# Performance work log

Measured on AMD Instinct MI355X. Metric: run time of the kernel, lower is better.

## Reference

```python
import jax, jax.numpy as jnp
import numpy as np

N = 100_000      # nodes
E = 500_000      # bonds
DN = 128         # dim_node_embedding
DB = 64          # dim_bond_embedding
NTOK = 4         # num_bond_token
DIN = 2 * DN + 2 * DB  # 384
LEAKY = 0.001
LN_EPS = 1e-5
DIST_MAX = 20.0
STEP = 0.5


def _lrelu(v):
    return jnp.where(v >= 0, v, LEAKY * v)


def _layernorm(v, w, b):
    m = v.mean(-1, keepdims=True)
    var = ((v - m) ** 2).mean(-1, keepdims=True)
    return (v - m) / jnp.sqrt(var + LN_EPS) * w + b


def setup_inputs() -> dict:
    key = jax.random.key(0)
    ks = jax.random.split(key, 20)
    x = jax.random.normal(ks[0], (N, 3), dtype=jnp.float32) * 3.0
    pos = jax.random.normal(ks[1], (N, 3), dtype=jnp.float32)
    node_embedding = jax.random.normal(ks[2], (N, DN), dtype=jnp.float32)
    i0 = jax.random.randint(ks[3], (E,), 0, N)
    off = jax.random.randint(ks[4], (E,), 1, N)  # nonzero -> no self-bonds
    bond_index = jnp.stack([i0, (i0 + off) % N], axis=1).astype(jnp.int32)
    bond_types = jax.random.randint(ks[5], (E,), 0, NTOK).astype(jnp.int32)
    s = 0.02
    params = dict(
        bond_emb=jax.random.normal(ks[6], (NTOK, DB), dtype=jnp.float32),
        W0=jax.random.normal(ks[7], (DIN, DN), dtype=jnp.float32) * s,
        b0=jnp.zeros((DN,), jnp.float32),
        W1=jax.random.normal(ks[8], (DN, DN), dtype=jnp.float32) * s,
        b1=jnp.zeros((DN,), jnp.float32),
        ln1_w=jnp.ones((DN,), jnp.float32),
        ln1_b=jnp.zeros((DN,), jnp.float32),
        W2=jax.random.normal(ks[9], (DN, DN), dtype=jnp.float32) * s,
        b2=jnp.zeros((DN,), jnp.float32),
        ln2_w=jnp.ones((DN,), jnp.float32),
        ln2_b=jnp.zeros((DN,), jnp.float32),
        Wo=jax.random.normal(ks[10], (DN, 2), dtype=jnp.float32) * s,
        bo=jnp.zeros((2,), jnp.float32),
    )
    return dict(x=x, pos=pos, node_embedding=node_embedding,
                bond_index=bond_index, bond_types=bond_types, **params)


def reference(x, pos, node_embedding, bond_index, bond_types,
              bond_emb, W0, b0, W1, b1, ln1_w, ln1_b,
              W2, b2, ln2_w, ln2_b, Wo, bo):
    i = bond_index[:, 0]
    j = bond_index[:, 1]

    # ---- BondLength geometry ----
    diff = x[i] - x[j]                                   # [E,3]
    dist = jnp.linalg.norm(diff, axis=-1, keepdims=True)  # [E,1]
    u = diff / dist                                       # [E,3] unit j->i? (i-j)/d
    direction = jnp.stack([u, -u], axis=-1)               # [E,3,2]

    # ---- Smearing (gaussian RBF + overflow bin, normalized) ----
    offset = jnp.linspace(0.0, DIST_MAX, DB - 1, dtype=jnp.float32)  # [63]
    delta = DIST_MAX / (DB - 2)
    coeff = -0.5 / (delta * delta)
    rbf = jnp.exp(coeff * (dist - offset) ** 2)            # [E,63]
    ovf = (dist >= DIST_MAX).astype(x.dtype)               # [E,1]
    smear = jnp.concatenate([rbf, ovf], axis=-1)           # [E,64]
    smear = smear / smear.sum(axis=-1, keepdims=True)

    # ---- Edge MLP (LeakyMLP, num_layer=2, dim_end=2) ----
    feat = jnp.concatenate(
        [node_embedding[i], node_embedding[j], bond_emb[bond_types], smear],
        axis=-1)                                           # [E,384]
    h = _lrelu(feat @ W0 + b0)
    h = _lrelu(_layernorm(h @ W1 + b1, ln1_w, ln1_b))
    h = _lrelu(_layernorm(h @ W2 + b2, ln2_w, ln2_b))
    force = h @ Wo + bo                                    # [E,2]

    # ---- position update (scatter-add) ----
    update = force[:, None, :] * direction                 # [E,3,2]
    pos = pos.at[i].add(STEP * update[..., 0])
    pos = pos.at[j].add(STEP * update[..., 1])
    return pos
```

## Files before the change

kernel.cpp:

```cpp
#include <hip/hip_runtime.h>
#include <stdint.h>

#define N_EDGES 500000
#define N_NODES 100000
#define PREP_NG 4
#define TBINS 1280

typedef __attribute__((ext_vector_type(8))) short short8;
typedef __attribute__((ext_vector_type(4))) float floatx4;
typedef __attribute__((ext_vector_type(2))) float f32x2;
typedef __attribute__((ext_vector_type(4))) unsigned int u32x4v;
typedef __attribute__((ext_vector_type(2))) int i32x2v;

__device__ __forceinline__ uint16_t f2bf(float f) {
  union { float f; uint32_t u; } cv; cv.f = f;
  uint32_t u = cv.u;
  return (uint16_t)((u + 0x7FFFu + ((u >> 16) & 1u)) >> 16);
}
__device__ __forceinline__ uint32_t pk2bf(float lo, float hi) {
  return __builtin_amdgcn_perm(__float_as_uint(hi), __float_as_uint(lo), 0x07060302u);
}
__device__ __forceinline__ uint16_t bftrunc(float f) {
  return (uint16_t)(__float_as_uint(f) >> 16);
}
__device__ __forceinline__ float lrelu(float v) { return fmaxf(v, 0.001f * v); }

__device__ __forceinline__ f32x2 unpk2(uint32_t u) {
  return (f32x2){ __uint_as_float(u << 16), __uint_as_float(u & 0xFFFF0000u) };
}
__device__ __forceinline__ uint32_t comp2(uint32_t a, uint32_t b, uint32_t t0, uint32_t t1,
                                          f32x2 w2) {
  f32x2 p  = unpk2(a) + unpk2(b);
  f32x2 v0 = unpk2(t0), v1 = unpk2(t1);
  f32x2 r  = p + (v0 + w2 * (v1 - v0));
  f32x2 rl = r * 0.001f;
  return pk2bf(fmaxf(r.x, rl.x), fmaxf(r.y, rl.y));
}
__device__ __forceinline__ floatx4 lrelu4(floatx4 v) {
  floatx4 w = v * 0.001f;
  v.x = fmaxf(v.x, w.x); v.y = fmaxf(v.y, w.y);
  v.z = fmaxf(v.z, w.z); v.w = fmaxf(v.w, w.w);
  return v;
}

__global__ void prep0_kernel(const float* __restrict__ W0, const float* __restrict__ b0,
                             const float* __restrict__ W1, const float* __restrict__ W2,
                             const float* __restrict__ bemb,
                             uint16_t* __restrict__ w0ab, uint16_t* __restrict__ w1f,
                             uint16_t* __restrict__ w2f, float* __restrict__ be0f,
                             const float* __restrict__ pos, float* __restrict__ out, int npos) {
  int id = blockIdx.x * 256 + threadIdx.x;
  if (id < 32768) {
    int f = id;
    int j = f & 7, lane = (f >> 3) & 63, ntt = (f >> 9) & 15, ks = f >> 13;
    int k = ks * 32 + (lane >> 4) * 8 + j;
    int row = (ntt < 8) ? k : (128 + k);
    int col = (ntt & 7) * 16 + (lane & 15);
    w0ab[f] = f2bf(W0[row * 128 + col]);
  } else if (id < 49152) {
    int f = id - 32768;
    int j = f & 7, lane = (f >> 3) & 63, nt = (f >> 9) & 7, ks = f >> 12;
    int k = ks * 32 + (lane >> 4) * 8 + j;
    w1f[f] = f2bf(W1[k * 128 + nt * 16 + (lane & 15)]);
  } else if (id < 65536) {
    int f = id - 49152;
    int j = f & 7, lane = (f >> 3) & 63, nt = (f >> 9) & 7, ks = f >> 12;
    int k = ks * 32 + (lane >> 4) * 8 + j;
    w2f[f] = f2bf(W2[k * 128 + nt * 16 + (lane & 15)]);
  } else if (id < 66048) {
    int t = id - 65536; int ty = t >> 7, n = t & 127;
    float s = b0[n];
    for (int kk = 0; kk < 64; ++kk) s += bemb[ty * 64 + kk] * W0[(256 + kk) * 128 + n];
    be0f[t] = s;
  } else if (id - 66048 < npos) {
    out[id - 66048] = pos[id - 66048];
  }
}

__global__ __attribute__((amdgpu_flat_work_group_size(256, 256)))
void prep_tp_kernel(const float* __restrict__ W0, const float* __restrict__ be0f,
                    uint16_t* __restrict__ T,
                    const float* __restrict__ nemb, const uint16_t* __restrict__ w0ab,
                    uint16_t* __restrict__ Pa, uint16_t* __restrict__ Pb) {
  __shared__ __align__(16) uint16_t aLds[4 * PREP_NG * 16 * 136];
  __shared__ float rbf[64];
  const int tid = threadIdx.x;

  if (blockIdx.x < TBINS) {
    int b = blockIdx.x;
    float dist = (float)b * (1.0f / 32.0f);
    const float delta = 20.0f / 62.0f;
    const float coeff = -0.5f / (delta * delta);
    if (tid < 64) {
      float v;
      if (tid < 63) { float d = dist - (float)tid * delta; v = __expf(coeff * d * d); }
      else v = (dist >= 20.0f) ? 1.0f : 0.0f;
      rbf[tid] = v;
    }
    __syncthreads();
    float sum = 0.0f;
    for (int k = 0; k < 64; ++k) sum += rbf[k];
    float rs = 1.0f / sum;
    for (int o = tid; o < 512; o += 256) {
      int ty = o >> 7, n = o & 127;
      float s = be0f[ty * 128 + n];
      for (int k = 0; k < 64; ++k) s += rbf[k] * rs * W0[(320 + k) * 128 + n];
      T[((size_t)(ty * TBINS + b)) * 128 + n] = f2bf(s);
    }
    return;
  }

  const int pblk = blockIdx.x - TBINS;
  const int lane = tid & 63;
  const int wave = tid >> 6;
  const int n15 = lane & 15;
  const int quad = lane >> 4;
  uint16_t* myA = aLds + wave * (PREP_NG * 16 * 136);
  const int base = pblk * (64 * PREP_NG) + wave * (16 * PREP_NG);

  {
    const int le = lane >> 2, sub = lane & 3;
#pragma unroll
    for (int it = 0; it < PREP_NG; ++it) {
      int r = base + it * 16 + le; if (r >= N_NODES) r = N_NODES - 1;
      const float4* src = (const float4*)(nemb + (size_t)r * 128);
#pragma unroll
      for (int g = 0; g < 4; ++g) {
        float4 a = src[sub * 8 + g * 2], b = src[sub * 8 + g * 2 + 1];
        uint4 pk;
        pk.x = pk2bf(a.x, a.y); pk.y = pk2bf(a.z, a.w);
        pk.z = pk2bf(b.x, b.y); pk.w = pk2bf(b.z, b.w);
        *(uint4*)(myA + (it * 16 + le) * 136 + sub * 32 + g * 8) = pk;
      }
    }
  }

  const short8* wfv = (const short8*)w0ab + lane;
#pragma unroll
  for (int q = 0; q < 4; ++q) {
    short8 bfr[16];
#pragma unroll
    for (int ks = 0; ks < 4; ++ks)
#pragma unroll
      for (int nq = 0; nq < 4; ++nq)
        bfr[ks * 4 + nq] = wfv[(ks * 16 + q * 4 + nq) * 64];
#pragma unroll
    for (int it = 0; it < PREP_NG; ++it) {
      floatx4 acc[4];
#pragma unroll
      for (int nq = 0; nq < 4; ++nq) acc[nq] = (floatx4){0.f, 0.f, 0.f, 0.f};
#pragma unroll
      for (int ks = 0; ks < 4; ++ks) {
        short8 a = *(const short8*)(myA + (it * 16 + n15) * 136 + ks * 32 + quad * 8);
#pragma unroll
        for (int nq = 0; nq < 4; ++nq)
          acc[nq] = __builtin_amdgcn_mfma_f32_16x16x32_bf16(a, bfr[ks * 4 + nq], acc[nq], 0, 0, 0);
      }
      uint16_t* dst = (q < 2) ? Pa : Pb;
      int cbase = ((q & 1) * 4) * 16 + n15;
#pragma unroll
      for (int nq = 0; nq < 4; ++nq) {
        int c = cbase + nq * 16;
#pragma unroll
        for (int r = 0; r < 4; ++r) {
          int row = base + it * 16 + quad * 4 + r;
          if (row < N_NODES) dst[(size_t)row * 128 + c] = bftrunc(acc[nq][r]);
        }
      }
    }
  }
}

__device__ __forceinline__ void gemm_g2(const uint16_t* __restrict__ wf,
                                        const uint16_t* aRow0, const uint16_t* aRow1,
                                        int lane, floatx4* acc0, floatx4* acc1) {
  short8 a0[4], a1[4];
#pragma unroll
  for (int ks = 0; ks < 4; ++ks) {
    a0[ks] = *(const short8*)(aRow0 + ks * 32);
    a1[ks] = *(const short8*)(aRow1 + ks * 32);
  }
  const short8* wv = (const short8*)wf + lane;
#pragma unroll
  for (int ks = 0; ks < 4; ++ks)
#pragma unroll
    for (int nt = 0; nt < 8; ++nt) {
      short8 b = wv[(ks * 8 + nt) * 64];
      acc0[nt] = __builtin_amdgcn_mfma_f32_16x16x32_bf16(a0[ks], b, acc0[nt], 0, 0, 0);
      acc1[nt] = __builtin_amdgcn_mfma_f32_16x16x32_bf16(a1[ks], b, acc1[nt], 0, 0, 0);
    }
}

__device__ __forceinline__ void epilogue1(floatx4* acc, uint16_t* hA, int n15, int quad,
                                          const float* __restrict__ b1,
                                          const float* __restrict__ ln1w,
                                          const float* __restrict__ ln1b) {
  float bv[8], wv[8], bb[8];
#pragma unroll
  for (int nt = 0; nt < 8; ++nt) {
    int col = nt * 16 + n15;
    bv[nt] = b1[col]; wv[nt] = ln1w[col]; bb[nt] = ln1b[col];
  }
  floatx4 s4 = {0.f, 0.f, 0.f, 0.f}, q4 = {0.f, 0.f, 0.f, 0.f};
#pragma unroll
  for (int nt = 0; nt < 8; ++nt) { floatx4 v = acc[nt] + bv[nt]; s4 += v; q4 += v * v; }
#pragma unroll
  for (int m = 1; m <= 8; m <<= 1) {
#pragma unroll
    for (int c = 0; c < 4; ++c) { s4[c] += __shfl_xor(s4[c], m); q4[c] += __shfl_xor(q4[c], m); }
  }
  floatx4 mean = s4 * (1.0f / 128.0f);
  floatx4 var = q4 * (1.0f / 128.0f) - mean * mean;
  floatx4 rstd;
  rstd.x = rsqrtf(var.x + 1e-5f); rstd.y = rsqrtf(var.y + 1e-5f);
  rstd.z = rsqrtf(var.z + 1e-5f); rstd.w = rsqrtf(var.w + 1e-5f);
#pragma unroll
  for (int nt = 0; nt < 8; ++nt) {
    floatx4 v = acc[nt] + bv[nt];
    floatx4 vn = lrelu4((v - mean) * (rstd * wv[nt]) + bb[nt]);
#pragma unroll
    for (int r = 0; r < 4; ++r)
      hA[(quad * 4 + r) * 136 + nt * 16 + n15] = bftrunc(vn[r]);
  }
}

__device__ __forceinline__ void epilogue2(floatx4* acc, int n15, int quad, int edge0, int gr0,
                                          const float (*u_lds)[3], const int (*ij_lds)[2],
                                          const float* __restrict__ b2,
                                          const float* __restrict__ ln2w,
                                          const float* __restrict__ ln2b,
                                          const float* __restrict__ Wo,
                                          const float* __restrict__ bo,
                                          float* __restrict__ out) {
  float bv[8], wv[8], bb[8], wo0[8], wo1[8];
#pragma unroll
  for (int nt = 0; nt < 8; ++nt) {
    int col = nt * 16 + n15;
    bv[nt] = b2[col]; wv[nt] = ln2w[col]; bb[nt] = ln2b[col];
    wo0[nt] = Wo[2 * col]; wo1[nt] = Wo[2 * col + 1];
  }
  floatx4 s4 = {0.f, 0.f, 0.f, 0.f}, q4 = {0.f, 0.f, 0.f, 0.f};
#pragma unroll
  for (int nt = 0; nt < 8; ++nt) { floatx4 v = acc[nt] + bv[nt]; s4 += v; q4 += v * v; }
#pragma unroll
  for (int m = 1; m <= 8; m <<= 1) {
#pragma unroll
    for (int c = 0; c < 4; ++c) { s4[c] += __shfl_xor(s4[c], m); q4[c] += __shfl_xor(q4[c], m); }
  }
  floatx4 mean = s4 * (1.0f / 128.0f);
  floatx4 var = q4 * (1.0f / 128.0f) - mean * mean;
  floatx4 rstd;
  rstd.x = rsqrtf(var.x + 1e-5f); rstd.y = rsqrtf(var.y + 1e-5f);
  rstd.z = rsqrtf(var.z + 1e-5f); rstd.w = rsqrtf(var.w + 1e-5f);
  floatx4 f0 = {0.f, 0.f, 0.f, 0.f}, f1 = {0.f, 0.f, 0.f, 0.f};
#pragma unroll
  for (int nt = 0; nt < 8; ++nt) {
    floatx4 v = acc[nt] + bv[nt];
    floatx4 vn = lrelu4((v - mean) * (rstd * wv[nt]) + bb[nt]);
    f0 += vn * wo0[nt];
    f1 += vn * wo1[nt];
  }
#pragma unroll
  for (int m = 1; m <= 8; m <<= 1) {
#pragma unroll
    for (int c = 0; c < 4; ++c) { f0[c] += __shfl_xor(f0[c], m); f1[c] += __shfl_xor(f1[c], m); }
  }
  if (n15 < 4) {
    int gr = gr0 + quad * 4 + n15;
    int ge2 = edge0 + quad * 4 + n15;
    if (ge2 < N_EDGES) {
      float F0 = (n15 == 0) ? f0.x : (n15 == 1) ? f0.y : (n15 == 2) ? f0.z : f0.w;
      float F1 = (n15 == 0) ? f1.x : (n15 == 1) ? f1.y : (n15 == 2) ? f1.z : f1.w;
      F0 += bo[0]; F1 += bo[1];
      float ux = u_lds[gr][0], uy = u_lds[gr][1], uz = u_lds[gr][2];
      int ii = ij_lds[gr][0], jj = ij_lds[gr][1];
      float c0 = 0.5f * F0;
      float c1 = -0.5f * F1;
      atomicAdd(out + 3 * ii,     c0 * ux);
      atomicAdd(out + 3 * ii + 1, c0 * uy);
      atomicAdd(out + 3 * ii + 2, c0 * uz);
      atomicAdd(out + 3 * jj,     c1 * ux);
      atomicAdd(out + 3 * jj + 1, c1 * uy);
      atomicAdd(out + 3 * jj + 2, c1 * uz);
    }
  }
}

__global__ __attribute__((amdgpu_flat_work_group_size(256, 256), amdgpu_waves_per_eu(2, 4)))
void bond_mlp_kernel(const float* __restrict__ x,
                     const int* __restrict__ bidx, const int* __restrict__ btyp,
                     const uint16_t* __restrict__ Pa, const uint16_t* __restrict__ Pb,
                     const uint16_t* __restrict__ Tt, const uint16_t* __restrict__ w1f,
                     const uint16_t* __restrict__ w2f,
                     const float* __restrict__ b1, const float* __restrict__ ln1w,
                     const float* __restrict__ ln1b,
                     const float* __restrict__ b2, const float* __restrict__ ln2w,
                     const float* __restrict__ ln2b,
                     const float* __restrict__ Wo, const float* __restrict__ bo,
                     float* __restrict__ out) {
  __shared__ __align__(16) uint16_t hA_all[8 * 16 * 136];
  __shared__ float u_lds[128][3];
  __shared__ int ij_lds[128][2];

  const int tid = threadIdx.x;
  const int lane = tid & 63;
  const int wave = tid >> 6;
  const int n15 = lane & 15;
  const int quad = lane >> 4;

  uint16_t* hA0 = hA_all + (wave * 2 + 0) * (16 * 136);
  uint16_t* hA1 = hA_all + (wave * 2 + 1) * (16 * 136);

#pragma unroll
  for (int g = 0; g < 2; ++g) {
    uint16_t* hA = (g == 0) ? hA0 : hA1;
    const int le = lane >> 2, sub = lane & 3;
    const int gr = wave * 32 + g * 16 + le;
    const int ge = blockIdx.x * 128 + gr;
    const bool valid = ge < N_EDGES;
    int vi = 0, vj = 0, bt = 0;
    if (valid) {
      i32x2v ij = __builtin_nontemporal_load((const i32x2v*)(bidx + 2 * ge));
      vi = ij.x; vj = ij.y;
      bt = __builtin_nontemporal_load(btyp + ge);
    }
    float dx, dy, dz;
    if (valid) {
      dx = x[3 * vi]     - x[3 * vj];
      dy = x[3 * vi + 1] - x[3 * vj + 1];
      dz = x[3 * vi + 2] - x[3 * vj + 2];
    } else { dx = 1.0f; dy = 0.0f; dz = 0.0f; }
    float dist = sqrtf(dx * dx + dy * dy + dz * dz);
    float rinv = 1.0f / dist;
    if (sub == 0) {
      u_lds[gr][0] = dx * rinv; u_lds[gr][1] = dy * rinv; u_lds[gr][2] = dz * rinv;
      ij_lds[gr][0] = vi; ij_lds[gr][1] = vj;
    }
    float fb = fminf(dist, 39.5f) * 32.0f;
    int bi = (int)fb;
    float w = fb - (float)bi;
    f32x2 w2 = {w, w};
    const u32x4v* pa = (const u32x4v*)(Pa + (size_t)vi * 128 + sub * 32);
    const u32x4v* pb = (const u32x4v*)(Pb + (size_t)vj * 128 + sub * 32);
    const uint16_t* trow = Tt + ((size_t)(bt * TBINS + bi)) * 128 + sub * 32;
    const u32x4v* t0p = (const u32x4v*)trow;
    const u32x4v* t1p = (const u32x4v*)(trow + 128);
#pragma unroll
    for (int gg = 0; gg < 4; ++gg) {
      u32x4v av = __builtin_nontemporal_load(pa + gg);
      u32x4v bw = __builtin_nontemporal_load(pb + gg);
      u32x4v t0 = t0p[gg];
      u32x4v t1 = t1p[gg];
      u32x4v pk;
      pk.x = comp2(av.x, bw.x, t0.x, t1.x, w2);
      pk.y = comp2(av.y, bw.y, t0.y, t1.y, w2);
      pk.z = comp2(av.z, bw.z, t0.z, t1.z, w2);
      pk.w = comp2(av.w, bw.w, t0.w, t1.w, w2);
      *(u32x4v*)(hA + le * 136 + sub * 32 + gg * 8) = pk;
    }
  }

  const uint16_t* aRow0 = hA0 + n15 * 136 + quad * 8;
  const uint16_t* aRow1 = hA1 + n15 * 136 + quad * 8;

  floatx4 acc0[8], acc1[8];
#pragma unroll
  for (int nt = 0; nt < 8; ++nt) {
    acc0[nt] = (floatx4){0.f, 0.f, 0.f, 0.f};
    acc1[nt] = (floatx4){0.f, 0.f, 0.f, 0.f};
  }
  gemm_g2(w1f, aRow0, aRow1, lane, acc0, acc1);

  epilogue1(acc0, hA0, n15, quad, b1, ln1w, ln1b);
  epilogue1(acc1, hA1, n15, quad, b1, ln1w, ln1b);

#pragma unroll
  for (int nt = 0; nt < 8; ++nt) {
    acc0[nt] = (floatx4){0.f, 0.f, 0.f, 0.f};
    acc1[nt] = (floatx4){0.f, 0.f, 0.f, 0.f};
  }
  gemm_g2(w2f, aRow0, aRow1, lane, acc0, acc1);

  const int e0 = blockIdx.x * 128 + wave * 32;
  epilogue2(acc0, n15, quad, e0,      wave * 32,      u_lds, ij_lds, b2, ln2w, ln2b, Wo, bo, out);
  epilogue2(acc1, n15, quad, e0 + 16, wave * 32 + 16, u_lds, ij_lds, b2, ln2w, ln2b, Wo, bo, out);
}

extern "C" void kernel_launch(void* const* d_in, const int* in_sizes, int n_in,
                              void* d_out, int out_size, void* d_ws, size_t ws_size,
                              hipStream_t stream) {
  const float* x    = (const float*)d_in[0];
  const float* pos  = (const float*)d_in[1];
  const float* nemb = (const float*)d_in[2];
  const int*   bidx = (const int*)d_in[3];
  const int*   btyp = (const int*)d_in[4];
  const float* bemb = (const float*)d_in[5];
  const float* W0   = (const float*)d_in[6];
  const float* b0   = (const float*)d_in[7];
  const float* W1   = (const float*)d_in[8];
  const float* b1   = (const float*)d_in[9];
  const float* ln1w = (const float*)d_in[10];
  const float* ln1b = (const float*)d_in[11];
  const float* W2   = (const float*)d_in[12];
  const float* b2   = (const float*)d_in[13];
  const float* ln2w = (const float*)d_in[14];
  const float* ln2b = (const float*)d_in[15];
  const float* Wo   = (const float*)d_in[16];
  const float* bo   = (const float*)d_in[17];
  float* out = (float*)d_out;

  uint16_t* w0ab = (uint16_t*)d_ws;
  uint16_t* w1f  = w0ab + 32768;
  uint16_t* w2f  = w1f + 16384;
  float*    be0f = (float*)(w2f + 16384);
  uint16_t* Tt   = (uint16_t*)(be0f + 512);
  uint16_t* Pa   = Tt + (size_t)4 * TBINS * 128;
  uint16_t* Pb   = Pa + (size_t)N_NODES * 128;

  const int nblkP = (N_NODES + 64 * PREP_NG - 1) / (64 * PREP_NG);

  prep0_kernel<<<(66048 + out_size + 255) / 256, 256, 0, stream>>>(
      W0, b0, W1, W2, bemb, w0ab, w1f, w2f, be0f, pos, out, out_size);
  prep_tp_kernel<<<TBINS + nblkP, 256, 0, stream>>>(
      W0, be0f, Tt, nemb, w0ab, Pa, Pb);
  bond_mlp_kernel<<<(N_EDGES + 127) / 128, 256, 0, stream>>>(
      x, bidx, btyp, Pa, Pb, Tt, w1f, w2f,
      b1, ln1w, ln1b, b2, ln2w, ln2b, Wo, bo, out);
}
```

Before: 390.8 us.

## Use finer distance table with nearest lookup, one tile per wave, coalesced prep stores

Quadruples the distance-bin table resolution and replaces linear interpolation between two table rows with a nearest-bin lookup, so each edge reads one table row instead of two. The bond kernel now processes one 16-edge tile per wave, with 64 edges per block and an occupancy hint of 4 waves, instead of two tiles per wave. The node-projection prep stages its MFMA results through LDS so that global writes become coalesced 16-byte stores, and PREP_NG is halved. Nontemporal loads are dropped. The trade-offs are more table-build blocks and an approximation error that now depends on the finer bin spacing.

```diff
diff --git a/kernel.cpp b/kernel.cpp
--- a/kernel.cpp
+++ b/kernel.cpp
@@ -3,14 +3,12 @@
 
 #define N_EDGES 500000
 #define N_NODES 100000
-#define PREP_NG 4
-#define TBINS 1280
+#define PREP_NG 2
+#define TBINS 5120
 
 typedef __attribute__((ext_vector_type(8))) short short8;
 typedef __attribute__((ext_vector_type(4))) float floatx4;
 typedef __attribute__((ext_vector_type(2))) float f32x2;
-typedef __attribute__((ext_vector_type(4))) unsigned int u32x4v;
-typedef __attribute__((ext_vector_type(2))) int i32x2v;
 
 __device__ __forceinline__ uint16_t f2bf(float f) {
   union { float f; uint32_t u; } cv; cv.f = f;
@@ -28,11 +26,8 @@
 __device__ __forceinline__ f32x2 unpk2(uint32_t u) {
   return (f32x2){ __uint_as_float(u << 16), __uint_as_float(u & 0xFFFF0000u) };
 }
-__device__ __forceinline__ uint32_t comp2(uint32_t a, uint32_t b, uint32_t t0, uint32_t t1,
-                                          f32x2 w2) {
-  f32x2 p  = unpk2(a) + unpk2(b);
-  f32x2 v0 = unpk2(t0), v1 = unpk2(t1);
-  f32x2 r  = p + (v0 + w2 * (v1 - v0));
+__device__ __forceinline__ uint32_t comp2n(uint32_t a, uint32_t b, uint32_t t) {
+  f32x2 r = unpk2(a) + unpk2(b) + unpk2(t);
   f32x2 rl = r * 0.001f;
   return pk2bf(fmaxf(r.x, rl.x), fmaxf(r.y, rl.y));
 }
@@ -83,12 +78,13 @@
                     const float* __restrict__ nemb, const uint16_t* __restrict__ w0ab,
                     uint16_t* __restrict__ Pa, uint16_t* __restrict__ Pb) {
   __shared__ __align__(16) uint16_t aLds[4 * PREP_NG * 16 * 136];
+  __shared__ __align__(16) uint16_t sS[4][16][72];
   __shared__ float rbf[64];
   const int tid = threadIdx.x;
 
   if (blockIdx.x < TBINS) {
     int b = blockIdx.x;
-    float dist = (float)b * (1.0f / 32.0f);
+    float dist = (float)b * (1.0f / 128.0f);
     const float delta = 20.0f / 62.0f;
     const float coeff = -0.5f / (delta * delta);
     if (tid < 64) {
@@ -136,6 +132,7 @@
   }
 
   const short8* wfv = (const short8*)w0ab + lane;
+  const int srow = lane >> 2, sch = lane & 3;
 #pragma unroll
   for (int q = 0; q < 4; ++q) {
     short8 bfr[16];
@@ -144,6 +141,8 @@
 #pragma unroll
       for (int nq = 0; nq < 4; ++nq)
         bfr[ks * 4 + nq] = wfv[(ks * 16 + q * 4 + nq) * 64];
+    uint16_t* dst = (q < 2) ? Pa : Pb;
+    const int cbase = (q & 1) * 64;
 #pragma unroll
     for (int it = 0; it < PREP_NG; ++it) {
       floatx4 acc[4];
@@ -156,137 +155,37 @@
         for (int nq = 0; nq < 4; ++nq)
           acc[nq] = __builtin_amdgcn_mfma_f32_16x16x32_bf16(a, bfr[ks * 4 + nq], acc[nq], 0, 0, 0);
       }
-      uint16_t* dst = (q < 2) ? Pa : Pb;
-      int cbase = ((q & 1) * 4) * 16 + n15;
-#pragma unroll
-      for (int nq = 0; nq < 4; ++nq) {
-        int c = cbase + nq * 16;
-#pragma unroll
-        for (int r = 0; r < 4; ++r) {
-          int row = base + it * 16 + quad * 4 + r;
-          if (row < N_NODES) dst[(size_t)row * 128 + c] = bftrunc(acc[nq][r]);
-        }
+#pragma unroll
+      for (int nq = 0; nq < 4; ++nq)
+#pragma unroll
+        for (int r = 0; r < 4; ++r)
+          sS[wave][quad * 4 + r][nq * 16 + n15] = bftrunc(acc[nq][r]);
+      int grow = base + it * 16 + srow;
+      if (grow < N_NODES) {
+        uint16_t* drow = dst + (size_t)grow * 128 + cbase;
+#pragma unroll
+        for (int h = 0; h < 2; ++h)
+          *(uint4*)(drow + (h * 4 + sch) * 8) =
+              *(const uint4*)&sS[wave][srow][(h * 4 + sch) * 8];
       }
     }
   }
 }
 
-__device__ __forceinline__ void gemm_g2(const uint16_t* __restrict__ wf,
-                                        const uint16_t* aRow0, const uint16_t* aRow1,
-                                        int lane, floatx4* acc0, floatx4* acc1) {
-  short8 a0[4], a1[4];
-#pragma unroll
-  for (int ks = 0; ks < 4; ++ks) {
-    a0[ks] = *(const short8*)(aRow0 + ks * 32);
-    a1[ks] = *(const short8*)(aRow1 + ks * 32);
-  }
+__device__ __forceinline__ void gemm_g(const uint16_t* __restrict__ wf, const uint16_t* aRow,
+                                       int lane, floatx4* acc) {
+  short8 a[4];
+#pragma unroll
+  for (int ks = 0; ks < 4; ++ks) a[ks] = *(const short8*)(aRow + ks * 32);
   const short8* wv = (const short8*)wf + lane;
 #pragma unroll
   for (int ks = 0; ks < 4; ++ks)
 #pragma unroll
-    for (int nt = 0; nt < 8; ++nt) {
-      short8 b = wv[(ks * 8 + nt) * 64];
-      acc0[nt] = __builtin_amdgcn_mfma_f32_16x16x32_bf16(a0[ks], b, acc0[nt], 0, 0, 0);
-      acc1[nt] = __builtin_amdgcn_mfma_f32_16x16x32_bf16(a1[ks], b, acc1[nt], 0, 0, 0);
-    }
-}
-
-__device__ __forceinline__ void epilogue1(floatx4* acc, uint16_t* hA, int n15, int quad,
-                                          const float* __restrict__ b1,
-                                          const float* __restrict__ ln1w,
-                                          const float* __restrict__ ln1b) {
-  float bv[8], wv[8], bb[8];
-#pragma unroll
-  for (int nt = 0; nt < 8; ++nt) {
-    int col = nt * 16 + n15;
-    bv[nt] = b1[col]; wv[nt] = ln1w[col]; bb[nt] = ln1b[col];
-  }
-  floatx4 s4 = {0.f, 0.f, 0.f, 0.f}, q4 = {0.f, 0.f, 0.f, 0.f};
-#pragma unroll
-  for (int nt = 0; nt < 8; ++nt) { floatx4 v = acc[nt] + bv[nt]; s4 += v; q4 += v * v; }
-#pragma unroll
-  for (int m = 1; m <= 8; m <<= 1) {
-#pragma unroll
-    for (int c = 0; c < 4; ++c) { s4[c] += __shfl_xor(s4[c], m); q4[c] += __shfl_xor(q4[c], m); }
-  }
-  floatx4 mean = s4 * (1.0f / 128.0f);
-  floatx4 var = q4 * (1.0f / 128.0f) - mean * mean;
-  floatx4 rstd;
-  rstd.x = rsqrtf(var.x + 1e-5f); rstd.y = rsqrtf(var.y + 1e-5f);
-  rstd.z = rsqrtf(var.z + 1e-5f); rstd.w = rsqrtf(var.w + 1e-5f);
-#pragma unroll
-  for (int nt = 0; nt < 8; ++nt) {
-    floatx4 v = acc[nt] + bv[nt];
-    floatx4 vn = lrelu4((v - mean) * (rstd * wv[nt]) + bb[nt]);
-#pragma unroll
-    for (int r = 0; r < 4; ++r)
-      hA[(quad * 4 + r) * 136 + nt * 16 + n15] = bftrunc(vn[r]);
-  }
-}
-
-__device__ __forceinline__ void epilogue2(floatx4* acc, int n15, int quad, int edge0, int gr0,
-                                          const float (*u_lds)[3], const int (*ij_lds)[2],
-                                          const float* __restrict__ b2,
-                                          const float* __restrict__ ln2w,
-                                          const float* __restrict__ ln2b,
-                                          const float* __restrict__ Wo,
-                                          const float* __restrict__ bo,
-                                          float* __restrict__ out) {
-  float bv[8], wv[8], bb[8], wo0[8], wo1[8];
-#pragma unroll
-  for (int nt = 0; nt < 8; ++nt) {
-    int col = nt * 16 + n15;
-    bv[nt] = b2[col]; wv[nt] = ln2w[col]; bb[nt] = ln2b[col];
-    wo0[nt] = Wo[2 * col]; wo1[nt] = Wo[2 * col + 1];
-  }
-  floatx4 s4 = {0.f, 0.f, 0.f, 0.f}, q4 = {0.f, 0.f, 0.f, 0.f};
-#pragma unroll
-  for (int nt = 0; nt < 8; ++nt) { floatx4 v = acc[nt] + bv[nt]; s4 += v; q4 += v * v; }
-#pragma unroll
-  for (int m = 1; m <= 8; m <<= 1) {
-#pragma unroll
-    for (int c = 0; c < 4; ++c) { s4[c] += __shfl_xor(s4[c], m); q4[c] += __shfl_xor(q4[c], m); }
-  }
-  floatx4 mean = s4 * (1.0f / 128.0f);
-  floatx4 var = q4 * (1.0f / 128.0f) - mean * mean;
-  floatx4 rstd;
-  rstd.x = rsqrtf(var.x + 1e-5f); rstd.y = rsqrtf(var.y + 1e-5f);
-  rstd.z = rsqrtf(var.z + 1e-5f); rstd.w = rsqrtf(var.w + 1e-5f);
-  floatx4 f0 = {0.f, 0.f, 0.f, 0.f}, f1 = {0.f, 0.f, 0.f, 0.f};
-#pragma unroll
-  for (int nt = 0; nt < 8; ++nt) {
-    floatx4 v = acc[nt] + bv[nt];
-    floatx4 vn = lrelu4((v - mean) * (rstd * wv[nt]) + bb[nt]);
-    f0 += vn * wo0[nt];
-    f1 += vn * wo1[nt];
-  }
-#pragma unroll
-  for (int m = 1; m <= 8; m <<= 1) {
-#pragma unroll
-    for (int c = 0; c < 4; ++c) { f0[c] += __shfl_xor(f0[c], m); f1[c] += __shfl_xor(f1[c], m); }
-  }
-  if (n15 < 4) {
-    int gr = gr0 + quad * 4 + n15;
-    int ge2 = edge0 + quad * 4 + n15;
-    if (ge2 < N_EDGES) {
-      float F0 = (n15 == 0) ? f0.x : (n15 == 1) ? f0.y : (n15 == 2) ? f0.z : f0.w;
-      float F1 = (n15 == 0) ? f1.x : (n15 == 1) ? f1.y : (n15 == 2) ? f1.z : f1.w;
-      F0 += bo[0]; F1 += bo[1];
-      float ux = u_lds[gr][0], uy = u_lds[gr][1], uz = u_lds[gr][2];
-      int ii = ij_lds[gr][0], jj = ij_lds[gr][1];
-      float c0 = 0.5f * F0;
-      float c1 = -0.5f * F1;
-      atomicAdd(out + 3 * ii,     c0 * ux);
-      atomicAdd(out + 3 * ii + 1, c0 * uy);
-      atomicAdd(out + 3 * ii + 2, c0 * uz);
-      atomicAdd(out + 3 * jj,     c1 * ux);
-      atomicAdd(out + 3 * jj + 1, c1 * uy);
-      atomicAdd(out + 3 * jj + 2, c1 * uz);
-    }
-  }
-}
-
-__global__ __attribute__((amdgpu_flat_work_group_size(256, 256), amdgpu_waves_per_eu(2, 4)))
+    for (int nt = 0; nt < 8; ++nt)
+      acc[nt] = __builtin_amdgcn_mfma_f32_16x16x32_bf16(a[ks], wv[(ks * 8 + nt) * 64], acc[nt], 0, 0, 0);
+}
+
+__global__ __attribute__((amdgpu_flat_work_group_size(256, 256), amdgpu_waves_per_eu(4)))
 void bond_mlp_kernel(const float* __restrict__ x,
                      const int* __restrict__ bidx, const int* __restrict__ btyp,
                      const uint16_t* __restrict__ Pa, const uint16_t* __restrict__ Pb,
@@ -298,9 +197,9 @@
                      const float* __restrict__ ln2b,
                      const float* __restrict__ Wo, const float* __restrict__ bo,
                      float* __restrict__ out) {
-  __shared__ __align__(16) uint16_t hA_all[8 * 16 * 136];
-  __shared__ float u_lds[128][3];
-  __shared__ int ij_lds[128][2];
+  __shared__ __align__(16) uint16_t hA_all[4 * 16 * 136];
+  __shared__ float u_lds[64][3];
+  __shared__ int ij_lds[64][2];
 
   const int tid = threadIdx.x;
   const int lane = tid & 63;
@@ -308,21 +207,18 @@
   const int n15 = lane & 15;
   const int quad = lane >> 4;
 
-  uint16_t* hA0 = hA_all + (wave * 2 + 0) * (16 * 136);
-  uint16_t* hA1 = hA_all + (wave * 2 + 1) * (16 * 136);
-
-#pragma unroll
-  for (int g = 0; g < 2; ++g) {
-    uint16_t* hA = (g == 0) ? hA0 : hA1;
+  uint16_t* hA = hA_all + wave * (16 * 136);
+
+  {
     const int le = lane >> 2, sub = lane & 3;
-    const int gr = wave * 32 + g * 16 + le;
-    const int ge = blockIdx.x * 128 + gr;
+    const int gr = wave * 16 + le;
+    const int ge = blockIdx.x * 64 + gr;
     const bool valid = ge < N_EDGES;
     int vi = 0, vj = 0, bt = 0;
     if (valid) {
-      i32x2v ij = __builtin_nontemporal_load((const i32x2v*)(bidx + 2 * ge));
+      int2 ij = *(const int2*)(bidx + 2 * ge);
       vi = ij.x; vj = ij.y;
-      bt = __builtin_nontemporal_load(btyp + ge);
+      bt = btyp[ge];
     }
     float dx, dy, dz;
     if (valid) {
@@ -336,54 +232,117 @@
       u_lds[gr][0] = dx * rinv; u_lds[gr][1] = dy * rinv; u_lds[gr][2] = dz * rinv;
       ij_lds[gr][0] = vi; ij_lds[gr][1] = vj;
     }
-    float fb = fminf(dist, 39.5f) * 32.0f;
-    int bi = (int)fb;
-    float w = fb - (float)bi;
-    f32x2 w2 = {w, w};
-    const u32x4v* pa = (const u32x4v*)(Pa + (size_t)vi * 128 + sub * 32);
-    const u32x4v* pb = (const u32x4v*)(Pb + (size_t)vj * 128 + sub * 32);
-    const uint16_t* trow = Tt + ((size_t)(bt * TBINS + bi)) * 128 + sub * 32;
-    const u32x4v* t0p = (const u32x4v*)trow;
-    const u32x4v* t1p = (const u32x4v*)(trow + 128);
-#pragma unroll
-    for (int gg = 0; gg < 4; ++gg) {
-      u32x4v av = __builtin_nontemporal_load(pa + gg);
-      u32x4v bw = __builtin_nontemporal_load(pb + gg);
-      u32x4v t0 = t0p[gg];
-      u32x4v t1 = t1p[gg];
-      u32x4v pk;
-      pk.x = comp2(av.x, bw.x, t0.x, t1.x, w2);
-      pk.y = comp2(av.y, bw.y, t0.y, t1.y, w2);
-      pk.z = comp2(av.z, bw.z, t0.z, t1.z, w2);
-      pk.w = comp2(av.w, bw.w, t0.w, t1.w, w2);
-      *(u32x4v*)(hA + le * 136 + sub * 32 + gg * 8) = pk;
-    }
-  }
-
-  const uint16_t* aRow0 = hA0 + n15 * 136 + quad * 8;
-  const uint16_t* aRow1 = hA1 + n15 * 136 + quad * 8;
-
-  floatx4 acc0[8], acc1[8];
-#pragma unroll
-  for (int nt = 0; nt < 8; ++nt) {
-    acc0[nt] = (floatx4){0.f, 0.f, 0.f, 0.f};
-    acc1[nt] = (floatx4){0.f, 0.f, 0.f, 0.f};
-  }
-  gemm_g2(w1f, aRow0, aRow1, lane, acc0, acc1);
-
-  epilogue1(acc0, hA0, n15, quad, b1, ln1w, ln1b);
-  epilogue1(acc1, hA1, n15, quad, b1, ln1w, ln1b);
-
-#pragma unroll
-  for (int nt = 0; nt < 8; ++nt) {
-    acc0[nt] = (floatx4){0.f, 0.f, 0.f, 0.f};
-    acc1[nt] = (floatx4){0.f, 0.f, 0.f, 0.f};
-  }
-  gemm_g2(w2f, aRow0, aRow1, lane, acc0, acc1);
-
-  const int e0 = blockIdx.x * 128 + wave * 32;
-  epilogue2(acc0, n15, quad, e0,      wave * 32,      u_lds, ij_lds, b2, ln2w, ln2b, Wo, bo, out);
-  epilogue2(acc1, n15, quad, e0 + 16, wave * 32 + 16, u_lds, ij_lds, b2, ln2w, ln2b, Wo, bo, out);
+    int bi = (int)(fminf(dist, 39.9f) * 128.0f + 0.5f);
+    const uint4* pa = (const uint4*)(Pa + (size_t)vi * 128 + sub * 32);
+    const uint4* pb = (const uint4*)(Pb + (size_t)vj * 128 + sub * 32);
+    const uint4* tp = (const uint4*)(Tt + ((size_t)(bt * TBINS + bi)) * 128 + sub * 32);
+#pragma unroll
+    for (int g = 0; g < 4; ++g) {
+      uint4 av = pa[g], bv = pb[g], tv = tp[g];
+      uint4 pk;
+      pk.x = comp2n(av.x, bv.x, tv.x);
+      pk.y = comp2n(av.y, bv.y, tv.y);
+      pk.z = comp2n(av.z, bv.z, tv.z);
+      pk.w = comp2n(av.w, bv.w, tv.w);
+      *(uint4*)(hA + le * 136 + sub * 32 + g * 8) = pk;
+    }
+  }
+
+  const uint16_t* aRow = hA + n15 * 136 + quad * 8;
+
+  floatx4 acc[8];
+#pragma unroll
+  for (int nt = 0; nt < 8; ++nt) acc[nt] = (floatx4){0.f, 0.f, 0.f, 0.f};
+  gemm_g(w1f, aRow, lane, acc);
+
+  {
+    float bv[8], wv[8], bb[8];
+#pragma unroll
+    for (int nt = 0; nt < 8; ++nt) {
+      int col = nt * 16 + n15;
+      bv[nt] = b1[col]; wv[nt] = ln1w[col]; bb[nt] = ln1b[col];
+    }
+    floatx4 s4 = {0.f, 0.f, 0.f, 0.f}, q4 = {0.f, 0.f, 0.f, 0.f};
+#pragma unroll
+    for (int nt = 0; nt < 8; ++nt) { floatx4 v = acc[nt] + bv[nt]; s4 += v; q4 += v * v; }
+#pragma unroll
+    for (int m = 1; m <= 8; m <<= 1) {
+#pragma unroll
+      for (int c = 0; c < 4; ++c) { s4[c] += __shfl_xor(s4[c], m); q4[c] += __shfl_xor(q4[c], m); }
+    }
+    floatx4 mean = s4 * (1.0f / 128.0f);
+    floatx4 var = q4 * (1.0f / 128.0f) - mean * mean;
+    floatx4 rstd;
+    rstd.x = rsqrtf(var.x + 1e-5f); rstd.y = rsqrtf(var.y + 1e-5f);
+    rstd.z = rsqrtf(var.z + 1e-5f); rstd.w = rsqrtf(var.w + 1e-5f);
+#pragma unroll
+    for (int nt = 0; nt < 8; ++nt) {
+      floatx4 v = acc[nt] + bv[nt];
+      floatx4 vn = lrelu4((v - mean) * (rstd * wv[nt]) + bb[nt]);
+#pragma unroll
+      for (int r = 0; r < 4; ++r)
+        hA[(quad * 4 + r) * 136 + nt * 16 + n15] = bftrunc(vn[r]);
+    }
+  }
+
+#pragma unroll
+  for (int nt = 0; nt < 8; ++nt) acc[nt] = (floatx4){0.f, 0.f, 0.f, 0.f};
+  gemm_g(w2f, aRow, lane, acc);
+
+  {
+    float bv[8], wv[8], bb[8], wo0[8], wo1[8];
+#pragma unroll
+    for (int nt = 0; nt < 8; ++nt) {
+      int col = nt * 16 + n15;
+      bv[nt] = b2[col]; wv[nt] = ln2w[col]; bb[nt] = ln2b[col];
+      wo0[nt] = Wo[2 * col]; wo1[nt] = Wo[2 * col + 1];
+    }
+    floatx4 s4 = {0.f, 0.f, 0.f, 0.f}, q4 = {0.f, 0.f, 0.f, 0.f};
+#pragma unroll
+    for (int nt = 0; nt < 8; ++nt) { floatx4 v = acc[nt] + bv[nt]; s4 += v; q4 += v * v; }
+#pragma unroll
+    for (int m = 1; m <= 8; m <<= 1) {
+#pragma unroll
+      for (int c = 0; c < 4; ++c) { s4[c] += __shfl_xor(s4[c], m); q4[c] += __shfl_xor(q4[c], m); }
+    }
+    floatx4 mean = s4 * (1.0f / 128.0f);
+    floatx4 var = q4 * (1.0f / 128.0f) - mean * mean;
+    floatx4 rstd;
+    rstd.x = rsqrtf(var.x + 1e-5f); rstd.y = rsqrtf(var.y + 1e-5f);
+    rstd.z = rsqrtf(var.z + 1e-5f); rstd.w = rsqrtf(var.w + 1e-5f);
+    floatx4 f0 = {0.f, 0.f, 0.f, 0.f}, f1 = {0.f, 0.f, 0.f, 0.f};
+#pragma unroll
+    for (int nt = 0; nt < 8; ++nt) {
+      floatx4 v = acc[nt] + bv[nt];
+      floatx4 vn = lrelu4((v - mean) * (rstd * wv[nt]) + bb[nt]);
+      f0 += vn * wo0[nt];
+      f1 += vn * wo1[nt];
+    }
+#pragma unroll
+    for (int m = 1; m <= 8; m <<= 1) {
+#pragma unroll
+      for (int c = 0; c < 4; ++c) { f0[c] += __shfl_xor(f0[c], m); f1[c] += __shfl_xor(f1[c], m); }
+    }
+    if (n15 < 4) {
+      int gr = wave * 16 + quad * 4 + n15;
+      int ge2 = blockIdx.x * 64 + gr;
+      if (ge2 < N_EDGES) {
+        float F0 = (n15 == 0) ? f0.x : (n15 == 1) ? f0.y : (n15 == 2) ? f0.z : f0.w;
+        float F1 = (n15 == 0) ? f1.x : (n15 == 1) ? f1.y : (n15 == 2) ? f1.z : f1.w;
+        F0 += bo[0]; F1 += bo[1];
+        float ux = u_lds[gr][0], uy = u_lds[gr][1], uz = u_lds[gr][2];
+        int ii = ij_lds[gr][0], jj = ij_lds[gr][1];
+        float c0 = 0.5f * F0;
+        float c1 = -0.5f * F1;
+        atomicAdd(out + 3 * ii,     c0 * ux);
+        atomicAdd(out + 3 * ii + 1, c0 * uy);
+        atomicAdd(out + 3 * ii + 2, c0 * uz);
+        atomicAdd(out + 3 * jj,     c1 * ux);
+        atomicAdd(out + 3 * jj + 1, c1 * uy);
+        atomicAdd(out + 3 * jj + 2, c1 * uz);
+      }
+    }
+  }
 }
 
 extern "C" void kernel_launch(void* const* d_in, const int* in_sizes, int n_in,
@@ -423,7 +382,7 @@
       W0, b0, W1, W2, bemb, w0ab, w1f, w2f, be0f, pos, out, out_size);
   prep_tp_kernel<<<TBINS + nblkP, 256, 0, stream>>>(
       W0, be0f, Tt, nemb, w0ab, Pa, Pb);
-  bond_mlp_kernel<<<(N_EDGES + 127) / 128, 256, 0, stream>>>(
+  bond_mlp_kernel<<<(N_EDGES + 63) / 64, 256, 0, stream>>>(
       x, bidx, btyp, Pa, Pb, Tt, w1f, w2f,
       b1, ln1w, ln1b, b2, ln2w, ln2b, Wo, bo, out);
 }
```

Measured after the change: 352.6 us. 1.11x faster.

## Stage prep GEMM output through LDS for coalesced stores, drop nontemporal loads

Applied to the files above, without the earlier changes.

The prep kernel now writes each MFMA output tile into a per-wave LDS staging buffer and then stores whole 16-byte row chunks to Pa/Pb, replacing scattered 2-byte global stores. PREP_NG is halved, which shrinks LDS use and makes smaller node groups per block. In the bond MLP kernel the nontemporal loads of indices and gathered Pa/Pb rows become ordinary cached loads, so repeated node rows can hit cache. The occupancy hint changes from waves_per_eu(2,4) to a minimum of 4, which may push register pressure into spills.

```diff
diff --git a/kernel.cpp b/kernel.cpp
--- a/kernel.cpp
+++ b/kernel.cpp
@@ -3,14 +3,12 @@
 
 #define N_EDGES 500000
 #define N_NODES 100000
-#define PREP_NG 4
+#define PREP_NG 2
 #define TBINS 1280
 
 typedef __attribute__((ext_vector_type(8))) short short8;
 typedef __attribute__((ext_vector_type(4))) float floatx4;
 typedef __attribute__((ext_vector_type(2))) float f32x2;
-typedef __attribute__((ext_vector_type(4))) unsigned int u32x4v;
-typedef __attribute__((ext_vector_type(2))) int i32x2v;
 
 __device__ __forceinline__ uint16_t f2bf(float f) {
   union { float f; uint32_t u; } cv; cv.f = f;
@@ -83,6 +81,7 @@
                     const float* __restrict__ nemb, const uint16_t* __restrict__ w0ab,
                     uint16_t* __restrict__ Pa, uint16_t* __restrict__ Pb) {
   __shared__ __align__(16) uint16_t aLds[4 * PREP_NG * 16 * 136];
+  __shared__ __align__(16) uint16_t sS[4][16][72];
   __shared__ float rbf[64];
   const int tid = threadIdx.x;
 
@@ -136,6 +135,7 @@
   }
 
   const short8* wfv = (const short8*)w0ab + lane;
+  const int srow = lane >> 2, sch = lane & 3;
 #pragma unroll
   for (int q = 0; q < 4; ++q) {
     short8 bfr[16];
@@ -144,6 +144,8 @@
 #pragma unroll
       for (int nq = 0; nq < 4; ++nq)
         bfr[ks * 4 + nq] = wfv[(ks * 16 + q * 4 + nq) * 64];
+    uint16_t* dst = (q < 2) ? Pa : Pb;
+    const int cbase = (q & 1) * 64;
 #pragma unroll
     for (int it = 0; it < PREP_NG; ++it) {
       floatx4 acc[4];
@@ -156,16 +158,18 @@
         for (int nq = 0; nq < 4; ++nq)
           acc[nq] = __builtin_amdgcn_mfma_f32_16x16x32_bf16(a, bfr[ks * 4 + nq], acc[nq], 0, 0, 0);
       }
-      uint16_t* dst = (q < 2) ? Pa : Pb;
-      int cbase = ((q & 1) * 4) * 16 + n15;
-#pragma unroll
-      for (int nq = 0; nq < 4; ++nq) {
-        int c = cbase + nq * 16;
-#pragma unroll
-        for (int r = 0; r < 4; ++r) {
-          int row = base + it * 16 + quad * 4 + r;
-          if (row < N_NODES) dst[(size_t)row * 128 + c] = bftrunc(acc[nq][r]);
-        }
+#pragma unroll
+      for (int nq = 0; nq < 4; ++nq)
+#pragma unroll
+        for (int r = 0; r < 4; ++r)
+          sS[wave][quad * 4 + r][nq * 16 + n15] = bftrunc(acc[nq][r]);
+      int grow = base + it * 16 + srow;
+      if (grow < N_NODES) {
+        uint16_t* drow = dst + (size_t)grow * 128 + cbase;
+#pragma unroll
+        for (int h = 0; h < 2; ++h)
+          *(uint4*)(drow + (h * 4 + sch) * 8) =
+              *(const uint4*)&sS[wave][srow][(h * 4 + sch) * 8];
       }
     }
   }
@@ -286,7 +290,7 @@
   }
 }
 
-__global__ __attribute__((amdgpu_flat_work_group_size(256, 256), amdgpu_waves_per_eu(2, 4)))
+__global__ __attribute__((amdgpu_flat_work_group_size(256, 256), amdgpu_waves_per_eu(4)))
 void bond_mlp_kernel(const float* __restrict__ x,
                      const int* __restrict__ bidx, const int* __restrict__ btyp,
                      const uint16_t* __restrict__ Pa, const uint16_t* __restrict__ Pb,
@@ -320,9 +324,9 @@
     const bool valid = ge < N_EDGES;
     int vi = 0, vj = 0, bt = 0;
     if (valid) {
-      i32x2v ij = __builtin_nontemporal_load((const i32x2v*)(bidx + 2 * ge));
+      int2 ij = *(const int2*)(bidx + 2 * ge);
       vi = ij.x; vj = ij.y;
-      bt = __builtin_nontemporal_load(btyp + ge);
+      bt = btyp[ge];
     }
     float dx, dy, dz;
     if (valid) {
@@ -340,23 +344,20 @@
     int bi = (int)fb;
     float w = fb - (float)bi;
     f32x2 w2 = {w, w};
-    const u32x4v* pa = (const u32x4v*)(Pa + (size_t)vi * 128 + sub * 32);
-    const u32x4v* pb = (const u32x4v*)(Pb + (size_t)vj * 128 + sub * 32);
+    const uint4* pa = (const uint4*)(Pa + (size_t)vi * 128 + sub * 32);
+    const uint4* pb = (const uint4*)(Pb + (size_t)vj * 128 + sub * 32);
     const uint16_t* trow = Tt + ((size_t)(bt * TBINS + bi)) * 128 + sub * 32;
-    const u32x4v* t0p = (const u32x4v*)trow;
-    const u32x4v* t1p = (const u32x4v*)(trow + 128);
+    const uint4* t0p = (const uint4*)trow;
+    const uint4* t1p = (const uint4*)(trow + 128);
 #pragma unroll
     for (int gg = 0; gg < 4; ++gg) {
-      u32x4v av = __builtin_nontemporal_load(pa + gg);
-      u32x4v bw = __builtin_nontemporal_load(pb + gg);
-      u32x4v t0 = t0p[gg];
-      u32x4v t1 = t1p[gg];
-      u32x4v pk;
-      pk.x = comp2(av.x, bw.x, t0.x, t1.x, w2);
-      pk.y = comp2(av.y, bw.y, t0.y, t1.y, w2);
-      pk.z = comp2(av.z, bw.z, t0.z, t1.z, w2);
-      pk.w = comp2(av.w, bw.w, t0.w, t1.w, w2);
-      *(u32x4v*)(hA + le * 136 + sub * 32 + gg * 8) = pk;
+      uint4 av = pa[gg], bv = pb[gg], t0 = t0p[gg], t1 = t1p[gg];
+      uint4 pk;
+      pk.x = comp2(av.x, bv.x, t0.x, t1.x, w2);
+      pk.y = comp2(av.y, bv.y, t0.y, t1.y, w2);
+      pk.z = comp2(av.z, bv.z, t0.z, t1.z, w2);
+      pk.w = comp2(av.w, bv.w, t0.w, t1.w, w2);
+      *(uint4*)(hA + le * 136 + sub * 32 + gg * 8) = pk;
     }
   }
 
```

Result: faster. 367.6 us (-5.9%).
